# Kernel optimization log

Measured on AMD Instinct MI355X. Metric: run time of the kernel, lower is better.

Reference implementation:

```python
import jax, jax.numpy as jnp
import numpy as np

B, T, D, H = 2, 2048, 1024, 16
HD = D // H  # 64
THETA = 10000.0


def _rope(x, pos):
    # x: (B,H,T,HD), pos: (T,) int
    half = HD // 2
    inv_freq = THETA ** (-jnp.arange(half, dtype=jnp.float32) * 2.0 / HD)  # (half,)
    ang = pos.astype(jnp.float32)[:, None] * inv_freq[None, :]  # (T, half)
    cos = jnp.cos(ang)[None, None]  # (1,1,T,half)
    sin = jnp.sin(ang)[None, None]
    x1 = x[..., 0::2]
    x2 = x[..., 1::2]
    r1 = x1 * cos - x2 * sin
    r2 = x1 * sin + x2 * cos
    return jnp.stack([r1, r2], axis=-1).reshape(x.shape)


def setup_inputs() -> dict:
    key = jax.random.key(0)
    ks = jax.random.split(key, 9)
    s = 0.02
    inp = {
        "x": jax.random.normal(ks[0], (B, T, D), dtype=jnp.float32),
        "token_positions": jnp.arange(T, dtype=jnp.int64),
        "wq": jax.random.normal(ks[1], (D, D), dtype=jnp.float32) * s,
        "bq": jnp.zeros((D,), dtype=jnp.float32),
        "wk": jax.random.normal(ks[2], (D, D), dtype=jnp.float32) * s,
        "bk": jnp.zeros((D,), dtype=jnp.float32),
        "wv": jax.random.normal(ks[3], (D, D), dtype=jnp.float32) * s,
        "bv": jnp.zeros((D,), dtype=jnp.float32),
        "wo": jax.random.normal(ks[4], (D, D), dtype=jnp.float32) * s,
        "bo": jnp.zeros((D,), dtype=jnp.float32),
    }
    return inp


def reference(x, token_positions, wq, bq, wk, bk, wv, bv, wo, bo):
    # Linear projections (torch Linear: x @ W.T + b)
    q = x @ wq.T + bq
    k = x @ wk.T + bk
    v = x @ wv.T + bv
    # (B,T,D) -> (B,H,T,HD)
    q = q.reshape(B, T, H, HD).transpose(0, 2, 1, 3)
    k = k.reshape(B, T, H, HD).transpose(0, 2, 1, 3)
    v = v.reshape(B, T, H, HD).transpose(0, 2, 1, 3)
    # RoPE on q and k
    q = _rope(q, token_positions)
    k = _rope(k, token_positions)
    # causal masked softmax attention
    scores = jnp.einsum('bhqd,bhkd->bhqk', q, k) / jnp.sqrt(jnp.float32(HD))
    keep = jnp.tril(jnp.ones((T, T), dtype=bool))  # keep mask (True = attend)
    scores = jnp.where(keep[None, None], scores, -jnp.inf)
    probs = jax.nn.softmax(scores, axis=-1)
    out = jnp.einsum('bhqk,bhkd->bhqd', probs, v)
    out = out.transpose(0, 2, 1, 3).reshape(B, T, D)
    return out @ wo.T + bo
```

## Files before the change

kernel.cpp:

```cpp
#include <hip/hip_runtime.h>
#include <hip/hip_bf16.h>

#define Bc 2
#define Tc 2048
#define Dc 1024
#define Hc 16
#define HDc 64

typedef __attribute__((ext_vector_type(4))) float f32x4;
typedef __attribute__((ext_vector_type(8))) short short8;
typedef __bf16 bf16x8 __attribute__((ext_vector_type(8)));

static __device__ __forceinline__ short f2bf(float f) {
  union { float f; unsigned u; } v; v.f = f;
  unsigned r = v.u + 0x7fffu + ((v.u >> 16) & 1u);
  return (short)(r >> 16);
}

static __device__ __forceinline__ f32x4 mfma16(bf16x8 a, bf16x8 b, f32x4 c) {
  return __builtin_amdgcn_mfma_f32_16x16x32_bf16(a, b, c, 0, 0, 0);
}

__global__ __launch_bounds__(256) void rope_tab_kernel(
    const int* __restrict__ tp, float2* __restrict__ tab)
{
  const int idx = blockIdx.x * 256 + threadIdx.x;
  const int t = idx >> 5, i = idx & 31;
  const float inv = expf((float)i * -0.2878231366242557f);
  float sn, cs;
  sincosf((float)tp[t] * inv, &sn, &cs);
  tab[idx] = make_float2(cs, sn);
}

template<int AMODE>
static __device__ __forceinline__ void gemm_core(
    const float* __restrict__ Af, const short* __restrict__ Ab,
    const float* __restrict__ W, const float* __restrict__ bias,
    int epi, const float2* __restrict__ rtab,
    short* __restrict__ outb, float* __restrict__ outf)
{
  __shared__ short As[64][40];
  __shared__ short Bs[64][40];
  const int tid = threadIdx.x;
  const int lane = tid & 63;
  const int w = tid >> 6;
  const int wr = w >> 1, wc = w & 1;
  const int nbase = blockIdx.x * 64;
  const int mbase = blockIdx.y * 64;
  const int srow = tid >> 2;
  const int scol = (tid & 3) * 8;
  const int fr = lane & 15, fq = lane >> 4, kg = fq * 8;

  f32x4 acc[2][2] = {};

  for (int k0 = 0; k0 < Dc; k0 += 32) {
    if (k0) __syncthreads();
    if (AMODE == 0) {
      const float* src = Af + (size_t)(mbase + srow) * Dc + k0 + scol;
      const float4 a0 = *(const float4*)src;
      const float4 a1 = *(const float4*)(src + 4);
      short* dst = &As[srow][scol];
      dst[0] = f2bf(a0.x); dst[1] = f2bf(a0.y); dst[2] = f2bf(a0.z); dst[3] = f2bf(a0.w);
      dst[4] = f2bf(a1.x); dst[5] = f2bf(a1.y); dst[6] = f2bf(a1.z); dst[7] = f2bf(a1.w);
    } else {
      *(short8*)&As[srow][scol] = *(const short8*)(Ab + (size_t)(mbase + srow) * Dc + k0 + scol);
    }
    {
      const float* src = W + (size_t)(nbase + srow) * Dc + k0 + scol;
      const float4 b0 = *(const float4*)src;
      const float4 b1 = *(const float4*)(src + 4);
      short* dst = &Bs[srow][scol];
      dst[0] = f2bf(b0.x); dst[1] = f2bf(b0.y); dst[2] = f2bf(b0.z); dst[3] = f2bf(b0.w);
      dst[4] = f2bf(b1.x); dst[5] = f2bf(b1.y); dst[6] = f2bf(b1.z); dst[7] = f2bf(b1.w);
    }
    __syncthreads();
    bf16x8 af[2], bfv[2];
    af[0] = *(const bf16x8*)&As[wr * 32 + fr][kg];
    af[1] = *(const bf16x8*)&As[wr * 32 + 16 + fr][kg];
    bfv[0] = *(const bf16x8*)&Bs[wc * 32 + fr][kg];
    bfv[1] = *(const bf16x8*)&Bs[wc * 32 + 16 + fr][kg];
    acc[0][0] = mfma16(af[0], bfv[0], acc[0][0]);
    acc[0][1] = mfma16(af[0], bfv[1], acc[0][1]);
    acc[1][0] = mfma16(af[1], bfv[0], acc[1][0]);
    acc[1][1] = mfma16(af[1], bfv[1], acc[1][1]);
  }

#pragma unroll
  for (int a2 = 0; a2 < 2; ++a2)
#pragma unroll
    for (int b2 = 0; b2 < 2; ++b2) {
      const int nl = wc * 32 + b2 * 16 + fr;
      const int n = nbase + nl;
      const float bv = bias[n];
#pragma unroll
      for (int r = 0; r < 4; ++r) {
        const int m = mbase + wr * 32 + a2 * 16 + fq * 4 + r;
        float v = acc[a2][b2][r] + bv;
        if (epi == 2) {
          outf[(size_t)m * Dc + n] = v;
        } else {
          const int t = m & (Tc - 1);
          const int bb = m >> 11;
          const int hd = n & 63, h = n >> 6;
          if (epi == 0) {
            const float nb = __shfl_xor(v, 1);
            const float2 cs = rtab[t * 32 + (hd >> 1)];
            v = (hd & 1) ? (nb * cs.y + v * cs.x) : (v * cs.x - nb * cs.y);
          }
          outb[(((size_t)bb * Hc + h) * Tc + t) * HDc + hd] = f2bf(v);
        }
      }
    }
}

__global__ __launch_bounds__(256) void qkv_kernel(
    const float* __restrict__ x,
    const float* __restrict__ wq, const float* __restrict__ bq,
    const float* __restrict__ wk, const float* __restrict__ bk,
    const float* __restrict__ wv, const float* __restrict__ bv,
    const float2* __restrict__ rtab,
    short* __restrict__ Qw, short* __restrict__ Kw, short* __restrict__ Vw)
{
  const int z = blockIdx.z;
  const float* W = (z == 0) ? wq : (z == 1) ? wk : wv;
  const float* bias = (z == 0) ? bq : (z == 1) ? bk : bv;
  short* outp = (z == 0) ? Qw : (z == 1) ? Kw : Vw;
  gemm_core<0>(x, nullptr, W, bias, (z < 2) ? 0 : 1, rtab, outp, nullptr);
}

__global__ __launch_bounds__(256) void out_kernel(
    const short* __restrict__ Ob, const float* __restrict__ wo,
    const float* __restrict__ bo, float* __restrict__ out)
{
  gemm_core<1>(nullptr, Ob, wo, bo, 2, nullptr, nullptr, out);
}

__global__ __launch_bounds__(256) void attn_kernel(
    const short* __restrict__ Qw, const short* __restrict__ Kw,
    const short* __restrict__ Vw, short* __restrict__ Ob)
{
  __shared__ short Ks[64][72];
  __shared__ short Vt[64][72];
  __shared__ short Ps[64][72];
  const int tid = threadIdx.x, lane = tid & 63, w = tid >> 6;
  const int bh = blockIdx.y, bb = bh >> 4, h = bh & 15;
  const int q0 = blockIdx.x * 64;
  const size_t base = (size_t)bh * Tc * HDc;
  const int fr = lane & 15, fq = lane >> 4, kg = fq * 8;

  bf16x8 qf[2];
  {
    const short* qrow = Qw + base + (size_t)(q0 + w * 16 + fr) * HDc;
    qf[0] = *(const bf16x8*)(qrow + kg);
    qf[1] = *(const bf16x8*)(qrow + 32 + kg);
  }

  f32x4 o[4] = {};
  float mrun[4] = {-1e30f, -1e30f, -1e30f, -1e30f};
  float lrun[4] = {0.f, 0.f, 0.f, 0.f};

  const int srow = tid >> 2;
  const int scol = (tid & 3) * 16;

  const int ntiles = blockIdx.x + 1;
  for (int kt = 0; kt < ntiles; ++kt) {
    const int kv0 = kt * 64;
    __syncthreads();
    {
      const short* ksrc = Kw + base + (size_t)(kv0 + srow) * HDc + scol;
      *(short8*)&Ks[srow][scol] = *(const short8*)ksrc;
      *(short8*)&Ks[srow][scol + 8] = *(const short8*)(ksrc + 8);
      const short* vsrc = Vw + base + (size_t)(kv0 + srow) * HDc + scol;
#pragma unroll
      for (int j = 0; j < 16; ++j) Vt[scol + j][srow] = vsrc[j];
    }
    __syncthreads();

    f32x4 s[4];
#pragma unroll
    for (int cf = 0; cf < 4; ++cf) {
      f32x4 acc = {};
      acc = mfma16(qf[0], *(const bf16x8*)&Ks[cf * 16 + fr][kg], acc);
      acc = mfma16(qf[1], *(const bf16x8*)&Ks[cf * 16 + fr][32 + kg], acc);
      s[cf] = acc * 0.125f;
    }
    if (kt == ntiles - 1) {
#pragma unroll
      for (int cf = 0; cf < 4; ++cf) {
        const int col = kv0 + cf * 16 + fr;
#pragma unroll
        for (int r = 0; r < 4; ++r) {
          const int row = q0 + w * 16 + fq * 4 + r;
          if (col > row) s[cf][r] = -1e30f;
        }
      }
    }
    float pm[4];
#pragma unroll
    for (int r = 0; r < 4; ++r)
      pm[r] = fmaxf(fmaxf(s[0][r], s[1][r]), fmaxf(s[2][r], s[3][r]));
#pragma unroll
    for (int d = 1; d < 16; d <<= 1)
#pragma unroll
      for (int r = 0; r < 4; ++r)
        pm[r] = fmaxf(pm[r], __shfl_xor(pm[r], d));
    float alpha[4], rs[4];
#pragma unroll
    for (int r = 0; r < 4; ++r) {
      const float mn = fmaxf(mrun[r], pm[r]);
      alpha[r] = __expf(mrun[r] - mn);
      mrun[r] = mn;
      rs[r] = 0.f;
    }
#pragma unroll
    for (int cf = 0; cf < 4; ++cf)
#pragma unroll
      for (int r = 0; r < 4; ++r) {
        const float p = __expf(s[cf][r] - mrun[r]);
        s[cf][r] = p;
        rs[r] += p;
      }
#pragma unroll
    for (int d = 1; d < 16; d <<= 1)
#pragma unroll
      for (int r = 0; r < 4; ++r)
        rs[r] += __shfl_xor(rs[r], d);
#pragma unroll
    for (int r = 0; r < 4; ++r)
      lrun[r] = lrun[r] * alpha[r] + rs[r];
#pragma unroll
    for (int df = 0; df < 4; ++df)
#pragma unroll
      for (int r = 0; r < 4; ++r)
        o[df][r] *= alpha[r];
#pragma unroll
    for (int cf = 0; cf < 4; ++cf)
#pragma unroll
      for (int r = 0; r < 4; ++r)
        Ps[w * 16 + fq * 4 + r][cf * 16 + fr] = f2bf(s[cf][r]);
    __syncthreads();
#pragma unroll
    for (int ks = 0; ks < 2; ++ks) {
      const bf16x8 pa = *(const bf16x8*)&Ps[w * 16 + fr][ks * 32 + kg];
#pragma unroll
      for (int df = 0; df < 4; ++df) {
        const bf16x8 vb = *(const bf16x8*)&Vt[df * 16 + fr][ks * 32 + kg];
        o[df] = mfma16(pa, vb, o[df]);
      }
    }
  }

#pragma unroll
  for (int df = 0; df < 4; ++df)
#pragma unroll
    for (int r = 0; r < 4; ++r) {
      const int t = q0 + w * 16 + fq * 4 + r;
      const float val = o[df][r] / lrun[r];
      Ob[((size_t)bb * Tc + t) * Dc + h * HDc + df * 16 + fr] = f2bf(val);
    }
}

extern "C" void kernel_launch(void* const* d_in, const int* in_sizes, int n_in,
                              void* d_out, int out_size, void* d_ws, size_t ws_size,
                              hipStream_t stream) {
  const float* x  = (const float*)d_in[0];
  const int*   tp = (const int*)d_in[1];
  const float* wq = (const float*)d_in[2];
  const float* bq = (const float*)d_in[3];
  const float* wk = (const float*)d_in[4];
  const float* bk = (const float*)d_in[5];
  const float* wv = (const float*)d_in[6];
  const float* bv = (const float*)d_in[7];
  const float* wo = (const float*)d_in[8];
  const float* bo = (const float*)d_in[9];
  float* out = (float*)d_out;

  char* ws = (char*)d_ws;
  short* Qw = (short*)(ws);
  short* Kw = (short*)(ws + (8u << 20));
  short* Vw = (short*)(ws + (16u << 20));
  short* Ob = (short*)(ws + (24u << 20));
  float2* rtab = (float2*)(ws + (24u << 20));

  dim3 blk(256);
  rope_tab_kernel<<<dim3(256), blk, 0, stream>>>(tp, rtab);
  qkv_kernel<<<dim3(16, 64, 3), blk, 0, stream>>>(x, wq, bq, wk, bk, wv, bv, rtab, Qw, Kw, Vw);
  attn_kernel<<<dim3(32, 32), blk, 0, stream>>>(Qw, Kw, Vw, Ob);
  out_kernel<<<dim3(16, 64), blk, 0, stream>>>(Ob, wo, bo, out);
}
```

Baseline: 332.5 us.

## Fuse QKV GEMM over shared A tile, pre-convert weights, reorder and swizzle attention

Adds a kernel that converts wq/wk/wv to bf16 once per call. The three projections then run in a single GEMM that loads and converts each x tile once and reuses it for Q, K and V, where before x was re-read and re-converted three times. The attention kernel now schedules the longest causal query tiles first and swizzles the Vt and Ps shared-memory layouts to reduce bank conflicts. In exchange there is an extra launch, more accumulator registers per thread, and three times the B tile in LDS for the QKV kernel.

```diff
diff --git a/kernel.cpp b/kernel.cpp
--- a/kernel.cpp
+++ b/kernel.cpp
@@ -19,6 +19,21 @@
 
 static __device__ __forceinline__ f32x4 mfma16(bf16x8 a, bf16x8 b, f32x4 c) {
   return __builtin_amdgcn_mfma_f32_16x16x32_bf16(a, b, c, 0, 0, 0);
+}
+
+__global__ __launch_bounds__(256) void wconv_kernel(
+    const float* __restrict__ wq, const float* __restrict__ wk,
+    const float* __restrict__ wv, short* __restrict__ Wb)
+{
+  const int z = blockIdx.y;
+  const float* src = (z == 0) ? wq : (z == 1) ? wk : wv;
+  const size_t i = ((size_t)blockIdx.x * 256 + threadIdx.x) * 8;
+  const float4 a0 = *(const float4*)(src + i);
+  const float4 a1 = *(const float4*)(src + i + 4);
+  short8 r;
+  r[0] = f2bf(a0.x); r[1] = f2bf(a0.y); r[2] = f2bf(a0.z); r[3] = f2bf(a0.w);
+  r[4] = f2bf(a1.x); r[5] = f2bf(a1.y); r[6] = f2bf(a1.z); r[7] = f2bf(a1.w);
+  *(short8*)(Wb + (size_t)z * 1048576 + i) = r;
 }
 
 __global__ __launch_bounds__(256) void rope_tab_kernel(
@@ -32,41 +47,96 @@
   tab[idx] = make_float2(cs, sn);
 }
 
-template<int AMODE>
-static __device__ __forceinline__ void gemm_core(
-    const float* __restrict__ Af, const short* __restrict__ Ab,
-    const float* __restrict__ W, const float* __restrict__ bias,
-    int epi, const float2* __restrict__ rtab,
-    short* __restrict__ outb, float* __restrict__ outf)
+__global__ __launch_bounds__(256) void qkv_kernel(
+    const float* __restrict__ x, const short* __restrict__ Wb,
+    const float* __restrict__ bq, const float* __restrict__ bk,
+    const float* __restrict__ bv, const float2* __restrict__ rtab,
+    short* __restrict__ Qw, short* __restrict__ Kw, short* __restrict__ Vw)
 {
   __shared__ short As[64][40];
-  __shared__ short Bs[64][40];
-  const int tid = threadIdx.x;
-  const int lane = tid & 63;
-  const int w = tid >> 6;
+  __shared__ short Bs[3][64][40];
+  const int tid = threadIdx.x, lane = tid & 63, w = tid >> 6;
   const int wr = w >> 1, wc = w & 1;
-  const int nbase = blockIdx.x * 64;
-  const int mbase = blockIdx.y * 64;
-  const int srow = tid >> 2;
-  const int scol = (tid & 3) * 8;
+  const int nbase = blockIdx.x * 64, mbase = blockIdx.y * 64;
+  const int srow = tid >> 2, scol = (tid & 3) * 8;
   const int fr = lane & 15, fq = lane >> 4, kg = fq * 8;
 
-  f32x4 acc[2][2] = {};
+  f32x4 acc[3][2][2] = {};
 
   for (int k0 = 0; k0 < Dc; k0 += 32) {
     if (k0) __syncthreads();
-    if (AMODE == 0) {
-      const float* src = Af + (size_t)(mbase + srow) * Dc + k0 + scol;
+    {
+      const float* src = x + (size_t)(mbase + srow) * Dc + k0 + scol;
       const float4 a0 = *(const float4*)src;
       const float4 a1 = *(const float4*)(src + 4);
       short* dst = &As[srow][scol];
       dst[0] = f2bf(a0.x); dst[1] = f2bf(a0.y); dst[2] = f2bf(a0.z); dst[3] = f2bf(a0.w);
       dst[4] = f2bf(a1.x); dst[5] = f2bf(a1.y); dst[6] = f2bf(a1.z); dst[7] = f2bf(a1.w);
-    } else {
-      *(short8*)&As[srow][scol] = *(const short8*)(Ab + (size_t)(mbase + srow) * Dc + k0 + scol);
-    }
+    }
+#pragma unroll
+    for (int z = 0; z < 3; ++z)
+      *(short8*)&Bs[z][srow][scol] =
+          *(const short8*)(Wb + (size_t)z * 1048576 + (size_t)(nbase + srow) * Dc + k0 + scol);
+    __syncthreads();
+    const bf16x8 af0 = *(const bf16x8*)&As[wr * 32 + fr][kg];
+    const bf16x8 af1 = *(const bf16x8*)&As[wr * 32 + 16 + fr][kg];
+#pragma unroll
+    for (int z = 0; z < 3; ++z) {
+      const bf16x8 b0 = *(const bf16x8*)&Bs[z][wc * 32 + fr][kg];
+      const bf16x8 b1 = *(const bf16x8*)&Bs[z][wc * 32 + 16 + fr][kg];
+      acc[z][0][0] = mfma16(af0, b0, acc[z][0][0]);
+      acc[z][0][1] = mfma16(af0, b1, acc[z][0][1]);
+      acc[z][1][0] = mfma16(af1, b0, acc[z][1][0]);
+      acc[z][1][1] = mfma16(af1, b1, acc[z][1][1]);
+    }
+  }
+
+#pragma unroll
+  for (int a2 = 0; a2 < 2; ++a2)
+#pragma unroll
+    for (int b2 = 0; b2 < 2; ++b2) {
+      const int n = nbase + wc * 32 + b2 * 16 + fr;
+      const float bi0 = bq[n], bi1 = bk[n], bi2 = bv[n];
+      const int hd = n & 63, h = n >> 6;
+#pragma unroll
+      for (int r = 0; r < 4; ++r) {
+        const int m = mbase + wr * 32 + a2 * 16 + fq * 4 + r;
+        const int t = m & (Tc - 1);
+        const int bbi = m >> 11;
+        const size_t oidx = (((size_t)bbi * Hc + h) * Tc + t) * HDc + hd;
+        const float2 cs = rtab[t * 32 + (hd >> 1)];
+        float v0 = acc[0][a2][b2][r] + bi0;
+        float v1 = acc[1][a2][b2][r] + bi1;
+        const float n0 = __shfl_xor(v0, 1);
+        const float n1 = __shfl_xor(v1, 1);
+        v0 = (hd & 1) ? (n0 * cs.y + v0 * cs.x) : (v0 * cs.x - n0 * cs.y);
+        v1 = (hd & 1) ? (n1 * cs.y + v1 * cs.x) : (v1 * cs.x - n1 * cs.y);
+        Qw[oidx] = f2bf(v0);
+        Kw[oidx] = f2bf(v1);
+        Vw[oidx] = f2bf(acc[2][a2][b2][r] + bi2);
+      }
+    }
+}
+
+__global__ __launch_bounds__(256) void out_kernel(
+    const short* __restrict__ Ob, const float* __restrict__ wo,
+    const float* __restrict__ bo, float* __restrict__ out)
+{
+  __shared__ short As[64][40];
+  __shared__ short Bs[64][40];
+  const int tid = threadIdx.x, lane = tid & 63, w = tid >> 6;
+  const int wr = w >> 1, wc = w & 1;
+  const int nbase = blockIdx.x * 64, mbase = blockIdx.y * 64;
+  const int srow = tid >> 2, scol = (tid & 3) * 8;
+  const int fr = lane & 15, fq = lane >> 4, kg = fq * 8;
+
+  f32x4 acc[2][2] = {};
+
+  for (int k0 = 0; k0 < Dc; k0 += 32) {
+    if (k0) __syncthreads();
+    *(short8*)&As[srow][scol] = *(const short8*)(Ob + (size_t)(mbase + srow) * Dc + k0 + scol);
     {
-      const float* src = W + (size_t)(nbase + srow) * Dc + k0 + scol;
+      const float* src = wo + (size_t)(nbase + srow) * Dc + k0 + scol;
       const float4 b0 = *(const float4*)src;
       const float4 b1 = *(const float4*)(src + 4);
       short* dst = &Bs[srow][scol];
@@ -74,65 +144,28 @@
       dst[4] = f2bf(b1.x); dst[5] = f2bf(b1.y); dst[6] = f2bf(b1.z); dst[7] = f2bf(b1.w);
     }
     __syncthreads();
-    bf16x8 af[2], bfv[2];
-    af[0] = *(const bf16x8*)&As[wr * 32 + fr][kg];
-    af[1] = *(const bf16x8*)&As[wr * 32 + 16 + fr][kg];
-    bfv[0] = *(const bf16x8*)&Bs[wc * 32 + fr][kg];
-    bfv[1] = *(const bf16x8*)&Bs[wc * 32 + 16 + fr][kg];
-    acc[0][0] = mfma16(af[0], bfv[0], acc[0][0]);
-    acc[0][1] = mfma16(af[0], bfv[1], acc[0][1]);
-    acc[1][0] = mfma16(af[1], bfv[0], acc[1][0]);
-    acc[1][1] = mfma16(af[1], bfv[1], acc[1][1]);
+    const bf16x8 af0 = *(const bf16x8*)&As[wr * 32 + fr][kg];
+    const bf16x8 af1 = *(const bf16x8*)&As[wr * 32 + 16 + fr][kg];
+    const bf16x8 b0 = *(const bf16x8*)&Bs[wc * 32 + fr][kg];
+    const bf16x8 b1 = *(const bf16x8*)&Bs[wc * 32 + 16 + fr][kg];
+    acc[0][0] = mfma16(af0, b0, acc[0][0]);
+    acc[0][1] = mfma16(af0, b1, acc[0][1]);
+    acc[1][0] = mfma16(af1, b0, acc[1][0]);
+    acc[1][1] = mfma16(af1, b1, acc[1][1]);
   }
 
 #pragma unroll
   for (int a2 = 0; a2 < 2; ++a2)
 #pragma unroll
     for (int b2 = 0; b2 < 2; ++b2) {
-      const int nl = wc * 32 + b2 * 16 + fr;
-      const int n = nbase + nl;
-      const float bv = bias[n];
+      const int n = nbase + wc * 32 + b2 * 16 + fr;
+      const float bv = bo[n];
 #pragma unroll
       for (int r = 0; r < 4; ++r) {
         const int m = mbase + wr * 32 + a2 * 16 + fq * 4 + r;
-        float v = acc[a2][b2][r] + bv;
-        if (epi == 2) {
-          outf[(size_t)m * Dc + n] = v;
-        } else {
-          const int t = m & (Tc - 1);
-          const int bb = m >> 11;
-          const int hd = n & 63, h = n >> 6;
-          if (epi == 0) {
-            const float nb = __shfl_xor(v, 1);
-            const float2 cs = rtab[t * 32 + (hd >> 1)];
-            v = (hd & 1) ? (nb * cs.y + v * cs.x) : (v * cs.x - nb * cs.y);
-          }
-          outb[(((size_t)bb * Hc + h) * Tc + t) * HDc + hd] = f2bf(v);
-        }
-      }
-    }
-}
-
-__global__ __launch_bounds__(256) void qkv_kernel(
-    const float* __restrict__ x,
-    const float* __restrict__ wq, const float* __restrict__ bq,
-    const float* __restrict__ wk, const float* __restrict__ bk,
-    const float* __restrict__ wv, const float* __restrict__ bv,
-    const float2* __restrict__ rtab,
-    short* __restrict__ Qw, short* __restrict__ Kw, short* __restrict__ Vw)
-{
-  const int z = blockIdx.z;
-  const float* W = (z == 0) ? wq : (z == 1) ? wk : wv;
-  const float* bias = (z == 0) ? bq : (z == 1) ? bk : bv;
-  short* outp = (z == 0) ? Qw : (z == 1) ? Kw : Vw;
-  gemm_core<0>(x, nullptr, W, bias, (z < 2) ? 0 : 1, rtab, outp, nullptr);
-}
-
-__global__ __launch_bounds__(256) void out_kernel(
-    const short* __restrict__ Ob, const float* __restrict__ wo,
-    const float* __restrict__ bo, float* __restrict__ out)
-{
-  gemm_core<1>(nullptr, Ob, wo, bo, 2, nullptr, nullptr, out);
+        out[(size_t)m * Dc + n] = acc[a2][b2][r] + bv;
+      }
+    }
 }
 
 __global__ __launch_bounds__(256) void attn_kernel(
@@ -144,7 +177,8 @@
   __shared__ short Ps[64][72];
   const int tid = threadIdx.x, lane = tid & 63, w = tid >> 6;
   const int bh = blockIdx.y, bb = bh >> 4, h = bh & 15;
-  const int q0 = blockIdx.x * 64;
+  const int qt = (int)gridDim.x - 1 - blockIdx.x;
+  const int q0 = qt * 64;
   const size_t base = (size_t)bh * Tc * HDc;
   const int fr = lane & 15, fq = lane >> 4, kg = fq * 8;
 
@@ -162,7 +196,7 @@
   const int srow = tid >> 2;
   const int scol = (tid & 3) * 16;
 
-  const int ntiles = blockIdx.x + 1;
+  const int ntiles = qt + 1;
   for (int kt = 0; kt < ntiles; ++kt) {
     const int kv0 = kt * 64;
     __syncthreads();
@@ -172,7 +206,10 @@
       *(short8*)&Ks[srow][scol + 8] = *(const short8*)(ksrc + 8);
       const short* vsrc = Vw + base + (size_t)(kv0 + srow) * HDc + scol;
 #pragma unroll
-      for (int j = 0; j < 16; ++j) Vt[scol + j][srow] = vsrc[j];
+      for (int j = 0; j < 16; ++j) {
+        const int row = scol + j;
+        Vt[row][(srow + (row & 56)) & 63] = vsrc[j];
+      }
     }
     __syncthreads();
 
@@ -233,18 +270,26 @@
 #pragma unroll
       for (int r = 0; r < 4; ++r)
         o[df][r] *= alpha[r];
-#pragma unroll
-    for (int cf = 0; cf < 4; ++cf)
-#pragma unroll
-      for (int r = 0; r < 4; ++r)
-        Ps[w * 16 + fq * 4 + r][cf * 16 + fr] = f2bf(s[cf][r]);
+    {
+      const int rowxor = (4 * w + fq) & 7;
+#pragma unroll
+      for (int cf = 0; cf < 4; ++cf) {
+        const int cblk = 2 * cf + (fr >> 3);
+        const int colp = (((cblk ^ rowxor) << 3) + (fr & 7));
+#pragma unroll
+        for (int r = 0; r < 4; ++r)
+          Ps[w * 16 + fq * 4 + r][colp] = f2bf(s[cf][r]);
+      }
+    }
     __syncthreads();
 #pragma unroll
     for (int ks = 0; ks < 2; ++ks) {
-      const bf16x8 pa = *(const bf16x8*)&Ps[w * 16 + fr][ks * 32 + kg];
+      const int prow = w * 16 + fr;
+      const bf16x8 pa = *(const bf16x8*)&Ps[prow][((4 * ks + fq) ^ ((prow >> 2) & 7)) << 3];
 #pragma unroll
       for (int df = 0; df < 4; ++df) {
-        const bf16x8 vb = *(const bf16x8*)&Vt[df * 16 + fr][ks * 32 + kg];
+        const int vr = df * 16 + fr;
+        const bf16x8 vb = *(const bf16x8*)&Vt[vr][(ks * 32 + kg + (vr & 56)) & 63];
         o[df] = mfma16(pa, vb, o[df]);
       }
     }
@@ -280,11 +325,13 @@
   short* Kw = (short*)(ws + (8u << 20));
   short* Vw = (short*)(ws + (16u << 20));
   short* Ob = (short*)(ws + (24u << 20));
-  float2* rtab = (float2*)(ws + (24u << 20));
+  short*  Wb   = (short*)(ws + (24u << 20));
+  float2* rtab = (float2*)(ws + (30u << 20));
 
   dim3 blk(256);
+  wconv_kernel<<<dim3(512, 3), blk, 0, stream>>>(wq, wk, wv, Wb);
   rope_tab_kernel<<<dim3(256), blk, 0, stream>>>(tp, rtab);
-  qkv_kernel<<<dim3(16, 64, 3), blk, 0, stream>>>(x, wq, bq, wk, bk, wv, bv, rtab, Qw, Kw, Vw);
+  qkv_kernel<<<dim3(16, 64), blk, 0, stream>>>(x, Wb, bq, bk, bv, rtab, Qw, Kw, Vw);
   attn_kernel<<<dim3(32, 32), blk, 0, stream>>>(Qw, Kw, Vw, Ob);
   out_kernel<<<dim3(16, 64), blk, 0, stream>>>(Ob, wo, bo, out);
 }
```

After: 310.8 us. 1.07x faster.
